# Kernel optimization log

Measured on AMD Instinct MI355X. Metric: run time of the kernel, lower is better.

## Reference

```python
import jax, jax.numpy as jnp
import numpy as np

NUM_HEADS = 16


def setup_inputs() -> dict:
    key = jax.random.key(0)
    k1, k2, k3, k4, k5 = jax.random.split(key, 5)
    B, N, C = 4, 1370, 1024
    s = 0.02
    return {
        "tokens": jax.random.normal(k1, (B, N, C), jnp.float32),
        "qkv_w": jax.random.normal(k2, (3 * C, C), jnp.float32) * s,
        "qkv_b": jax.random.normal(k3, (3 * C,), jnp.float32) * s,
        "proj_w": jax.random.normal(k4, (C, C), jnp.float32) * s,
        "proj_b": jax.random.normal(k5, (C,), jnp.float32) * s,
    }


def reference(tokens, qkv_w, qkv_b, proj_w, proj_b):
    B, N, C = tokens.shape
    H = NUM_HEADS
    c = C // H
    scale = c ** (-0.5)
    # qkv projection: [B,N,3C] -> [3,B,H,N,c]
    qkv = tokens @ qkv_w.T + qkv_b
    qkv = qkv.reshape(B, N, 3, H, c).transpose(2, 0, 3, 1, 4)
    q, k, v = qkv[0], qkv[1], qkv[2]
    q = q * scale
    attn = jnp.einsum("bhqc,bhkc->bhqk", q, k)  # [B,H,N,N]
    w = jax.nn.softmax(attn, axis=-1)
    out = jnp.einsum("bhqk,bhkc->bhqc", w, v)  # [B,H,N,c]
    out = out.transpose(0, 2, 1, 3).reshape(B, N, C)
    return out @ proj_w.T + proj_b
```

## Files before the change

kernel.cpp:

```cpp
#include <hip/hip_runtime.h>
#include <hip/hip_bf16.h>

typedef short s16x8 __attribute__((ext_vector_type(8)));
typedef float f32x4 __attribute__((ext_vector_type(4)));
typedef float f32x16 __attribute__((ext_vector_type(16)));
typedef unsigned short u16;
typedef unsigned int   u32;
typedef u16 u16x4 __attribute__((ext_vector_type(4)));

#define SEQ  1370
#define CH   1024
#define NH   16
#define HD   64
#define BN   5480
#define MPAD 5504
#define NPAD 1408
#define NQT  43
#define NKT64 22

#define QSCALE 0.18033688f


__device__ __forceinline__ u16 f2bf(float f){
  union { float f; unsigned u; } v; v.f = f;
  unsigned u = v.u;
  return (u16)((u + 0x7FFFu + ((u >> 16) & 1u)) >> 16);
}

__device__ __forceinline__ u32 cvt_pk_bf16(float lo, float hi){
  u32 r;
  asm("v_cvt_pk_bf16_f32 %0, %1, %2" : "=v"(r) : "v"(lo), "v"(hi));
  return r;
}

#define GLOAD16(gp, lp) __builtin_amdgcn_global_load_lds( \
    (const __attribute__((address_space(1))) void*)(gp), \
    (__attribute__((address_space(3))) void*)(lp), 16, 0, 0)

__global__ __launch_bounds__(256) void k_cast_tokens(const float* __restrict__ in, u16* __restrict__ out){
  int i = blockIdx.x * 256 + threadIdx.x;
  if(i >= MPAD*CH) return;
  int row = i >> 10;
  out[i] = (row < BN) ? f2bf(in[i]) : (u16)0;
}

__global__ __launch_bounds__(256) void k_cast(const float* __restrict__ in, u16* __restrict__ out, int n){
  int i = blockIdx.x * 256 + threadIdx.x;
  if(i < n) out[i] = f2bf(in[i]);
}

template<int MODE, int NT>
__global__ __launch_bounds__(256,2) void k_gemm128(
    const u16* __restrict__ A, const u16* __restrict__ Bw, const float* __restrict__ bias,
    u16* __restrict__ q, u16* __restrict__ kk_, u16* __restrict__ vv, float* __restrict__ out)
{
  constexpr int NF = NT/32;
  __shared__ u16 As[2][128*64];
  __shared__ u16 Bs[2][NT*64];
  const int t = threadIdx.x;
  const int lane = t & 63;
  const int w = t >> 6;
  const int wm = w >> 1, wn = w & 1;
  const int g = lane >> 4, lr = lane & 15;

  const int bid = blockIdx.x;
  const int xcd = bid & 7, idx = bid >> 3;
  const int xr = xcd & 3, yr = xcd >> 2;
  constexpr int YLOC = (MODE == 0) ? 12 : 8;
  const int x = xr*11 + idx % 11;
  const int y = yr*YLOC + idx / 11;
  if(x >= MPAD/128) return;
  const int m0 = x*128, n0 = y*NT;

  const int swc = ((t & 7) ^ ((t >> 3) & 7)) * 8;
  const u16* ga0 = A  + (size_t)(m0 + (t >> 3)) * 1024 + swc;
  const u16* gb0 = Bw + (size_t)(n0 + (t >> 3)) * 1024 + swc;

#define STAGE_G(K0, CB) { \
  _Pragma("unroll") \
  for(int j=0;j<4;j++) GLOAD16(ga0 + (K0) + j*32*1024, &As[CB][j*2048 + w*512]); \
  _Pragma("unroll") \
  for(int j=0;j<NF;j++) GLOAD16(gb0 + (K0) + j*32*1024, &Bs[CB][j*2048 + w*512]); }

  f32x4 z = {0.f,0.f,0.f,0.f};
  f32x4 acc[4][NF];
#pragma unroll
  for(int mf=0;mf<4;mf++)
#pragma unroll
    for(int nf=0;nf<NF;nf++) acc[mf][nf] = z;

  STAGE_G(0, 0);
  __syncthreads();
  for(int k0 = 0; k0 < 1024; k0 += 64){
    const int cur = (k0 >> 6) & 1;
    if(k0 + 64 < 1024) STAGE_G(k0 + 64, cur^1);
#pragma unroll
    for(int kk=0; kk<2; kk++){
      s16x8 af[4], bf[NF];
#pragma unroll
      for(int mf = 0; mf < 4; mf++)
        af[mf] = *reinterpret_cast<const s16x8*>(&As[cur][(wm*64 + mf*16 + lr)*64 + ((kk*4+g) ^ (lr&7))*8]);
#pragma unroll
      for(int nf = 0; nf < NF; nf++)
        bf[nf] = *reinterpret_cast<const s16x8*>(&Bs[cur][(wn*16*NF + nf*16 + lr)*64 + ((kk*4+g) ^ (lr&7))*8]);
#pragma unroll
      for(int mf = 0; mf < 4; mf++)
#pragma unroll
        for(int nf = 0; nf < NF; nf++)
          acc[mf][nf] = __builtin_amdgcn_mfma_f32_16x16x32_bf16(af[mf], bf[nf], acc[mf][nf], 0,0,0);
    }
    __syncthreads();
  }

#pragma unroll
  for(int mf = 0; mf < 4; mf++){
#pragma unroll
    for(int nf = 0; nf < NF; nf++){
      int colc = n0 + wn*16*NF + nf*16 + lr;
      float bb = bias[colc];
#pragma unroll
      for(int r = 0; r < 4; r++){
        int row = m0 + wm*64 + mf*16 + g*4 + r;
        if(row >= BN) continue;
        float v = acc[mf][nf][r] + bb;
        if constexpr (MODE == 0){
          int b = row / SEQ, n = row - b*SEQ;
          int tt = colc >> 10, h = (colc >> 6) & 15, cc = colc & 63;
          int bh = b*NH + h;
          if(tt == 2){
            int ktv = n >> 6, kh = (n >> 4) & 3, hiv = (n >> 3) & 1, e = n & 7;
            int dtv = cc >> 5, colr = cc & 31;
            vv[(size_t)((((bh*22 + ktv)*4 + kh)*2 + dtv)*2 + hiv)*256 + colr*8 + e] = f2bf(v);
          } else {
            int gg = n >> 5, colr = n & 31;
            int dtv = cc >> 4, hiq = (cc >> 3) & 1, e = cc & 7;
            size_t fidx = (size_t)(((bh*44 + gg)*4 + dtv)*2 + hiq)*256 + colr*8 + e;
            if(tt == 0) q  [fidx] = f2bf(v * QSCALE);
            else        kk_[fidx] = f2bf(v);
          }
        } else {
          out[(size_t)row * CH + colc] = v;
        }
      }
    }
  }
}

__global__ __launch_bounds__(256,3) void k_attn7(
    const u16* __restrict__ Qf, const u16* __restrict__ Kf,
    const u16* __restrict__ Vf, u16* __restrict__ O)
{
  __shared__ u16 Kl[2][4096];
  __shared__ u16 Vl[2][4096];
  const int bid = blockIdx.x;
  const int swz = (bid & 7)*88 + (bid >> 3);
  const int bh = swz / 11;
  const int qg = swz - bh*11;
  const int w = threadIdx.x >> 6;
  int qt = qg*4 + w;
  const bool wr = (qt < NQT);
  if(!wr) qt = NQT - 1;
  const int lane = threadIdx.x & 63;
  const int col = lane & 31;
  const int hi  = lane >> 5;
  const int n0  = qt * 32;
  const int lofs = hi*256 + col*8;

  s16x8 qf[4];
  {
    const u16* qfb = Qf + (size_t)(bh*44 + qt)*2048 + lofs;
#pragma unroll
    for(int dt=0; dt<4; dt++)
      qf[dt] = *reinterpret_cast<const s16x8*>(qfb + dt*512);
  }
  const u16* kfb = Kf + (size_t)bh*44*2048;
  const u16* vfb = Vf + (size_t)bh*22*4096;

#define STAGE_T(KT, CB) { \
  const u16* gk_ = kfb + (size_t)(KT)*4096 + w*1024 + lane*8; \
  const u16* gv_ = vfb + (size_t)(KT)*4096 + w*1024 + lane*8; \
  GLOAD16(gk_,       &Kl[CB][w*1024]); \
  GLOAD16(gk_ + 512, &Kl[CB][w*1024 + 512]); \
  GLOAD16(gv_,       &Vl[CB][w*1024]); \
  GLOAD16(gv_ + 512, &Vl[CB][w*1024 + 512]); }

  f32x16 accO[2];
#pragma unroll
  for(int i=0;i<16;i++){ accO[0][i]=0.f; accO[1][i]=0.f; }
  float m_run = -1e30f, l_run = 0.f;

  STAGE_T(0, 0);
  asm volatile("s_waitcnt vmcnt(0)" ::: "memory");
  __builtin_amdgcn_s_barrier();

  for(int kt = 0; kt < NKT64; kt++){
    const int kj0 = kt * 64;
    const int cur = kt & 1;
    if(kt + 1 < NKT64) STAGE_T(kt + 1, cur^1);
    f32x16 St[2];
    __builtin_amdgcn_s_setprio(1);
#pragma unroll
    for(int s=0;s<2;s++){
#pragma unroll
      for(int i=0;i<16;i++) St[s][i]=0.f;
#pragma unroll
      for(int dt=0;dt<4;dt++){
        s16x8 kf = *reinterpret_cast<const s16x8*>(&Kl[cur][s*2048 + dt*512 + lofs]);
        St[s] = __builtin_amdgcn_mfma_f32_32x32x16_bf16(kf, qf[dt], St[s], 0,0,0);
      }
    }
    __builtin_amdgcn_s_setprio(0);
    float p[32];
    if(kj0 + 64 <= SEQ){
#pragma unroll
      for(int i=0;i<32;i++) p[i] = St[i>>4][i&15];
    } else {
#pragma unroll
      for(int s=0;s<2;s++)
#pragma unroll
        for(int r=0;r<16;r++){
          int k = kj0 + s*32 + (r&3) + 8*(r>>2) + 4*hi;
          p[s*16+r] = (k < SEQ) ? St[s][r] : -1e30f;
        }
    }
    float red[16];
#pragma unroll
    for(int i=0;i<16;i++) red[i] = fmaxf(p[i], p[i+16]);
#pragma unroll
    for(int s2=8;s2>=1;s2>>=1)
#pragma unroll
      for(int i=0;i<8;i++) if(i<s2) red[i] = fmaxf(red[i], red[i+s2]);
    float mx = fmaxf(red[0], __shfl_xor(red[0], 32));
    if(!__all(mx <= m_run + 8.f)){
      float mnew = fmaxf(m_run, mx);
      float alpha = exp2f(m_run - mnew);
      m_run = mnew;
      l_run *= alpha;
#pragma unroll
      for(int i=0;i<16;i++){ accO[0][i]*=alpha; accO[1][i]*=alpha; }
    }
#pragma unroll
    for(int i=0;i<32;i++) p[i] = exp2f(p[i] - m_run);
    float sr[16];
#pragma unroll
    for(int i=0;i<16;i++) sr[i] = p[i] + p[i+16];
#pragma unroll
    for(int s2=8;s2>=1;s2>>=1)
#pragma unroll
      for(int i=0;i<8;i++) if(i<s2) sr[i] += sr[i+s2];
    l_run += sr[0] + __shfl_xor(sr[0], 32);
    union PF { u32 w[4]; s16x8 v; } pf[4];
#pragma unroll
    for(int s=0;s<2;s++){
#pragma unroll
      for(int hh=0; hh<2; hh++){
        const int b0 = s*16 + hh*8;
        u32 w0 = cvt_pk_bf16(p[b0+0], p[b0+1]);
        u32 w1 = cvt_pk_bf16(p[b0+2], p[b0+3]);
        u32 w2 = cvt_pk_bf16(p[b0+4], p[b0+5]);
        u32 w3 = cvt_pk_bf16(p[b0+6], p[b0+7]);
        auto r02 = __builtin_amdgcn_permlane32_swap(w0, w2, false, false);
        auto r13 = __builtin_amdgcn_permlane32_swap(w1, w3, false, false);
        pf[s*2+hh].w[0] = r02[0];
        pf[s*2+hh].w[1] = r13[0];
        pf[s*2+hh].w[2] = r02[1];
        pf[s*2+hh].w[3] = r13[1];
      }
    }
    __builtin_amdgcn_s_setprio(1);
#pragma unroll
    for(int kh=0; kh<4; kh++)
#pragma unroll
      for(int dt=0; dt<2; dt++){
        s16x8 vf = *reinterpret_cast<const s16x8*>(&Vl[cur][(kh*2+dt)*512 + lofs]);
        accO[dt] = __builtin_amdgcn_mfma_f32_32x32x16_bf16(vf, pf[kh].v, accO[dt], 0,0,0);
      }
    __builtin_amdgcn_s_setprio(0);
    asm volatile("s_waitcnt vmcnt(0)" ::: "memory");
    __builtin_amdgcn_s_barrier();
  }

  const int n = n0 + col;
  if(wr && n < SEQ){
    float inv = 1.0f / l_run;
    const int b = bh >> 4, h = bh & 15;
    u16* orow = O + ((size_t)(b*SEQ + n))*CH + h*HD;
#pragma unroll
    for(int dt=0; dt<2; dt++)
#pragma unroll
      for(int qd=0; qd<4; qd++){
        u16x4 ov;
#pragma unroll
        for(int j=0;j<4;j++) ov[j] = f2bf(accO[dt][qd*4+j]*inv);
        *reinterpret_cast<u16x4*>(orow + dt*32 + qd*8 + hi*4) = ov;
      }
  }
}

extern "C" void kernel_launch(void* const* d_in, const int* in_sizes, int n_in,
                              void* d_out, int out_size, void* d_ws, size_t ws_size,
                              hipStream_t stream)
{
  const float* tokens = (const float*)d_in[0];
  const float* qkv_w  = (const float*)d_in[1];
  const float* qkv_b  = (const float*)d_in[2];
  const float* proj_w = (const float*)d_in[3];
  const float* proj_b = (const float*)d_in[4];
  float* out = (float*)d_out;

  char* ws = (char*)d_ws;
  u16* Xbf   = (u16*)(ws);
  u16* Wqkv  = (u16*)(ws + 11272192);
  u16* Wproj = (u16*)(ws + 17563648);
  u16* Qfb   = (u16*)(ws + 19660800);
  u16* Kfb   = (u16*)(ws + 31195136);
  u16* Vfb   = (u16*)(ws + 42729472);
  u16* AttO  = (u16*)(ws + 65798144);

  k_cast_tokens<<<dim3((MPAD*CH)/256), 256, 0, stream>>>(tokens, Xbf);
  k_cast<<<dim3((3*CH*CH)/256), 256, 0, stream>>>(qkv_w, Wqkv, 3*CH*CH);
  k_cast<<<dim3((CH*CH)/256),   256, 0, stream>>>(proj_w, Wproj, CH*CH);

  k_gemm128<0,128><<<dim3(1056), 256, 0, stream>>>(Xbf, Wqkv, qkv_b, Qfb, Kfb, Vfb, nullptr);
  k_attn7<<<dim3(704), 256, 0, stream>>>(Qfb, Kfb, Vfb, AttO);
  k_gemm128<1,64><<<dim3(704), 256, 0, stream>>>(AttO, Wproj, proj_b, nullptr, nullptr, nullptr, out);
}
```

Before: 184.9 us.

## Single-buffer GEMM LDS staging and compute softmax row sums with MFMA

The projection GEMMs drop double-buffered LDS staging: each K step now loads one buffer, synchronizes, then computes. This halves the shared-memory footprint but gives up overlap between the next tile's loads and the current MFMAs. The attention kernel replaces the VALU tree reduction and cross-lane shuffle for the softmax denominator with an extra MFMA per key chunk against an all-ones bf16 operand. That moves work from the vector ALU to the matrix unit, at the cost of more MFMA issue and rounding the row sum from bf16 probabilities.

```diff
diff --git a/kernel.cpp b/kernel.cpp
--- a/kernel.cpp
+++ b/kernel.cpp
@@ -55,8 +55,8 @@
     u16* __restrict__ q, u16* __restrict__ kk_, u16* __restrict__ vv, float* __restrict__ out)
 {
   constexpr int NF = NT/32;
-  __shared__ u16 As[2][128*64];
-  __shared__ u16 Bs[2][NT*64];
+  __shared__ u16 As[128*64];
+  __shared__ u16 Bs[NT*64];
   const int t = threadIdx.x;
   const int lane = t & 63;
   const int w = t >> 6;
@@ -76,12 +76,6 @@
   const u16* ga0 = A  + (size_t)(m0 + (t >> 3)) * 1024 + swc;
   const u16* gb0 = Bw + (size_t)(n0 + (t >> 3)) * 1024 + swc;
 
-#define STAGE_G(K0, CB) { \
-  _Pragma("unroll") \
-  for(int j=0;j<4;j++) GLOAD16(ga0 + (K0) + j*32*1024, &As[CB][j*2048 + w*512]); \
-  _Pragma("unroll") \
-  for(int j=0;j<NF;j++) GLOAD16(gb0 + (K0) + j*32*1024, &Bs[CB][j*2048 + w*512]); }
-
   f32x4 z = {0.f,0.f,0.f,0.f};
   f32x4 acc[4][NF];
 #pragma unroll
@@ -89,20 +83,23 @@
 #pragma unroll
     for(int nf=0;nf<NF;nf++) acc[mf][nf] = z;
 
-  STAGE_G(0, 0);
-  __syncthreads();
   for(int k0 = 0; k0 < 1024; k0 += 64){
-    const int cur = (k0 >> 6) & 1;
-    if(k0 + 64 < 1024) STAGE_G(k0 + 64, cur^1);
+#pragma unroll
+    for(int j=0;j<4;j++)
+      GLOAD16(ga0 + k0 + j*32*1024, As + j*2048 + w*512);
+#pragma unroll
+    for(int j=0;j<NF;j++)
+      GLOAD16(gb0 + k0 + j*32*1024, Bs + j*2048 + w*512);
+    __syncthreads();
 #pragma unroll
     for(int kk=0; kk<2; kk++){
       s16x8 af[4], bf[NF];
 #pragma unroll
       for(int mf = 0; mf < 4; mf++)
-        af[mf] = *reinterpret_cast<const s16x8*>(&As[cur][(wm*64 + mf*16 + lr)*64 + ((kk*4+g) ^ (lr&7))*8]);
+        af[mf] = *reinterpret_cast<const s16x8*>(&As[(wm*64 + mf*16 + lr)*64 + ((kk*4+g) ^ (lr&7))*8]);
 #pragma unroll
       for(int nf = 0; nf < NF; nf++)
-        bf[nf] = *reinterpret_cast<const s16x8*>(&Bs[cur][(wn*16*NF + nf*16 + lr)*64 + ((kk*4+g) ^ (lr&7))*8]);
+        bf[nf] = *reinterpret_cast<const s16x8*>(&Bs[(wn*16*NF + nf*16 + lr)*64 + ((kk*4+g) ^ (lr&7))*8]);
 #pragma unroll
       for(int mf = 0; mf < 4; mf++)
 #pragma unroll
@@ -146,7 +143,7 @@
   }
 }
 
-__global__ __launch_bounds__(256,3) void k_attn7(
+__global__ __launch_bounds__(256,3) void k_attn8(
     const u16* __restrict__ Qf, const u16* __restrict__ Kf,
     const u16* __restrict__ Vf, u16* __restrict__ O)
 {
@@ -185,9 +182,12 @@
   GLOAD16(gv_ + 512, &Vl[CB][w*1024 + 512]); }
 
   f32x16 accO[2];
-#pragma unroll
-  for(int i=0;i<16;i++){ accO[0][i]=0.f; accO[1][i]=0.f; }
-  float m_run = -1e30f, l_run = 0.f;
+  f32x16 accL;
+#pragma unroll
+  for(int i=0;i<16;i++){ accO[0][i]=0.f; accO[1][i]=0.f; accL[i]=0.f; }
+  const s16x8 onesf = {(short)0x3F80,(short)0x3F80,(short)0x3F80,(short)0x3F80,
+                       (short)0x3F80,(short)0x3F80,(short)0x3F80,(short)0x3F80};
+  float m_run = -1e30f;
 
   STAGE_T(0, 0);
   asm volatile("s_waitcnt vmcnt(0)" ::: "memory");
@@ -235,20 +235,12 @@
       float mnew = fmaxf(m_run, mx);
       float alpha = exp2f(m_run - mnew);
       m_run = mnew;
-      l_run *= alpha;
+      accL[0] *= alpha;
 #pragma unroll
       for(int i=0;i<16;i++){ accO[0][i]*=alpha; accO[1][i]*=alpha; }
     }
 #pragma unroll
     for(int i=0;i<32;i++) p[i] = exp2f(p[i] - m_run);
-    float sr[16];
-#pragma unroll
-    for(int i=0;i<16;i++) sr[i] = p[i] + p[i+16];
-#pragma unroll
-    for(int s2=8;s2>=1;s2>>=1)
-#pragma unroll
-      for(int i=0;i<8;i++) if(i<s2) sr[i] += sr[i+s2];
-    l_run += sr[0] + __shfl_xor(sr[0], 32);
     union PF { u32 w[4]; s16x8 v; } pf[4];
 #pragma unroll
     for(int s=0;s<2;s++){
@@ -269,12 +261,14 @@
     }
     __builtin_amdgcn_s_setprio(1);
 #pragma unroll
-    for(int kh=0; kh<4; kh++)
+    for(int kh=0; kh<4; kh++){
 #pragma unroll
       for(int dt=0; dt<2; dt++){
         s16x8 vf = *reinterpret_cast<const s16x8*>(&Vl[cur][(kh*2+dt)*512 + lofs]);
         accO[dt] = __builtin_amdgcn_mfma_f32_32x32x16_bf16(vf, pf[kh].v, accO[dt], 0,0,0);
       }
+      accL = __builtin_amdgcn_mfma_f32_32x32x16_bf16(onesf, pf[kh].v, accL, 0,0,0);
+    }
     __builtin_amdgcn_s_setprio(0);
     asm volatile("s_waitcnt vmcnt(0)" ::: "memory");
     __builtin_amdgcn_s_barrier();
@@ -282,7 +276,7 @@
 
   const int n = n0 + col;
   if(wr && n < SEQ){
-    float inv = 1.0f / l_run;
+    float inv = 1.0f / accL[0];
     const int b = bh >> 4, h = bh & 15;
     u16* orow = O + ((size_t)(b*SEQ + n))*CH + h*HD;
 #pragma unroll
@@ -322,6 +316,6 @@
   k_cast<<<dim3((CH*CH)/256),   256, 0, stream>>>(proj_w, Wproj, CH*CH);
 
   k_gemm128<0,128><<<dim3(1056), 256, 0, stream>>>(Xbf, Wqkv, qkv_b, Qfb, Kfb, Vfb, nullptr);
-  k_attn7<<<dim3(704), 256, 0, stream>>>(Qfb, Kfb, Vfb, AttO);
+  k_attn8<<<dim3(704), 256, 0, stream>>>(Qfb, Kfb, Vfb, AttO);
   k_gemm128<1,64><<<dim3(704), 256, 0, stream>>>(AttO, Wproj, proj_b, nullptr, nullptr, nullptr, out);
 }
```

Measured after the change: 176.7 us. 1.05x faster.
